# Kernel optimization log

Hardware: AMD Instinct MI355X
Metric: run time of the kernel (lower is better)

The kernel has to match this reference:

```python
import jax, jax.numpy as jnp
import numpy as np

WINDOW = 2  # window_size

def _causal_window_conv(x, W, b):
    # x: [B,T,D_in], W: [WINDOW, D_in, D_out], b: [D_out]
    # equivalent to left-padding x by WINDOW-1 zeros and a 'valid' conv
    B, T, _ = x.shape
    xp = jnp.pad(x, ((0, 0), (WINDOW - 1, 0), (0, 0)))  # [B, T+WINDOW-1, D_in]
    out = b
    for k in range(WINDOW):
        out = out + jnp.einsum('btd,de->bte', xp[:, k:k + T], W[k])
    return out  # [B,T,D_out]

def setup_inputs() -> dict:
    key = jax.random.key(0)
    ks = jax.random.split(key, 4)
    B, T, Din, Dout = 8, 4096, 256, 256
    scale = 0.05
    x = jax.random.normal(ks[0], (B, T, Din), dtype=jnp.float32)
    W_z = jax.random.normal(ks[1], (WINDOW, Din, Dout), dtype=jnp.float32) * scale
    W_f = jax.random.normal(ks[2], (WINDOW, Din, Dout), dtype=jnp.float32) * scale
    W_o = jax.random.normal(ks[3], (WINDOW, Din, Dout), dtype=jnp.float32) * scale
    b_z = jnp.zeros((Dout,), dtype=jnp.float32)
    b_f = jnp.zeros((Dout,), dtype=jnp.float32)
    b_o = jnp.zeros((Dout,), dtype=jnp.float32)
    return {"x": x, "W_z": W_z, "W_f": W_f, "W_o": W_o,
            "b_z": b_z, "b_f": b_f, "b_o": b_o}

def reference(x, W_z, W_f, W_o, b_z, b_f, b_o):
    # QRNN with fo-pooling (Bradbury et al. 2016), return_sequences=True
    z = jnp.tanh(_causal_window_conv(x, W_z, b_z))          # [B,T,D]
    f = jax.nn.sigmoid(_causal_window_conv(x, W_f, b_f))    # [B,T,D]
    o = jax.nn.sigmoid(_causal_window_conv(x, W_o, b_o))    # [B,T,D]

    def step(c, zfo):
        z_t, f_t, o_t = zfo
        c = f_t * c + (1.0 - f_t) * z_t   # fo-pooling recurrence
        h = o_t * c
        return c, h

    c0 = jnp.zeros(z.shape[::2], dtype=z.dtype)  # [B,D]
    # time-major for scan
    zfo = (z.transpose(1, 0, 2), f.transpose(1, 0, 2), o.transpose(1, 0, 2))
    _, hs = jax.lax.scan(step, c0, zfo)
    return hs.transpose(1, 0, 2)  # [B,T,D]
```

## Files before the change

### kernel.cpp

```cpp
#include <hip/hip_runtime.h>
#include <hip/hip_bf16.h>
#include <hip/hip_fp16.h>

#define BDIM 8
#define TDIM 4096
#define DDIM 256
#define MDIM (BDIM * TDIM)
#define NCHUNK 256
#define LCHUNK (TDIM / NCHUNK)

typedef _Float16 f16x8 __attribute__((ext_vector_type(8)));
typedef _Float16 f16x4 __attribute__((ext_vector_type(4)));
typedef float f32x4 __attribute__((ext_vector_type(4)));

__device__ __forceinline__ float sigmoid_(float x) {
    return 1.0f / (1.0f + __expf(-x));
}
__device__ __forceinline__ float tanh_(float x) {
    return 2.0f / (1.0f + __expf(-2.0f * x)) - 1.0f;
}

#define GLOAD_LDS16(g, l)                                                    \
    __builtin_amdgcn_global_load_lds(                                        \
        (const __attribute__((address_space(1))) void*)(g),                  \
        (__attribute__((address_space(3))) void*)(l), 16, 0, 0)

__global__ __launch_bounds__(256) void prep(
    const float* __restrict__ x, _Float16* __restrict__ xpad,
    const float* __restrict__ Wz, const float* __restrict__ Wf,
    const float* __restrict__ Wo, _Float16* __restrict__ Wt) {
    const int bx = blockIdx.x;
    if (bx < 1536) {
        const int idx = bx * 256 + threadIdx.x;
        const int n = idx & 255;
        const int kin = (idx >> 8) & 255;
        const int w = (idx >> 16) & 1;
        const int g = idx >> 17;
        const float* W = (g == 0) ? Wz : (g == 1) ? Wf : Wo;
        const float v = W[(size_t)w * 65536 + (size_t)kin * 256 + n];
        Wt[((size_t)g * 256 + n) * 512 + w * 256 + kin] = (_Float16)v;
        return;
    }
    const int bxx = bx - 1536;
    const int b = bxx / 1025;
    const int tb = bxx - b * 1025;
    const int tp = tb * 4 + (threadIdx.x >> 6);
    const int q = threadIdx.x & 63;
    if (tp > TDIM) return;
    float4 v = make_float4(0.f, 0.f, 0.f, 0.f);
    if (tp > 0)
        v = *(const float4*)(x + ((size_t)b * TDIM + tp - 1) * DDIM + q * 4);
    f16x4 h;
    h[0] = (_Float16)v.x; h[1] = (_Float16)v.y;
    h[2] = (_Float16)v.z; h[3] = (_Float16)v.w;
    *(f16x4*)(xpad + ((size_t)b * (TDIM + 1) + tp) * DDIM + q * 4) = h;
}

__global__ __launch_bounds__(256, 2) void gates_mfma(
    const _Float16* __restrict__ xpad, const _Float16* __restrict__ Wt,
    const float* __restrict__ bz, const float* __restrict__ bfv,
    const float* __restrict__ bo,
    _Float16* __restrict__ zbuf, _Float16* __restrict__ fbuf,
    _Float16* __restrict__ obuf) {
    const int hw = blockIdx.x;
    const int logical = (hw & 7) * 192 + (hw >> 3);
    const int mblk = logical / 6;
    const int rem = logical - mblk * 6;
    const int gate = rem % 3;
    const int nblk = rem / 3;
    const int m0 = mblk * 128;
    const int n0 = nblk * 128;

    const int tid = threadIdx.x;
    const int lane = tid & 63;
    const int wave = tid >> 6;
    const int wr = wave >> 1;
    const int wc = wave & 1;

    __shared__ __align__(16) char smem[65536];

    const int s = wave * 64 + lane;
    const int r1 = s >> 3;
    const int kc = (((s & 7) ^ ((s >> 3) & 7))) * 8;

    const int b = m0 >> 12;
    const int t0 = m0 & (TDIM - 1);

    const _Float16* srcA =
        xpad + ((size_t)b * (TDIM + 1) + t0 + r1) * DDIM + kc;
    const _Float16* srcB = Wt + ((size_t)gate * 256 + n0 + r1) * 512 + kc;

#define STAGE_(slot, kt)                                                     \
    {                                                                        \
        char* dA = smem + (slot) * 32768 + wave * 1024;                      \
        char* dB = smem + (slot) * 32768 + 16384 + wave * 1024;              \
        GLOAD_LDS16(srcA + (kt) * 64, dA);                                   \
        GLOAD_LDS16(srcA + (kt) * 64 + 32 * DDIM, dA + 4096);                \
        GLOAD_LDS16(srcA + (kt) * 64 + 64 * DDIM, dA + 8192);                \
        GLOAD_LDS16(srcA + (kt) * 64 + 96 * DDIM, dA + 12288);               \
        GLOAD_LDS16(srcB + (kt) * 64, dB);                                   \
        GLOAD_LDS16(srcB + (kt) * 64 + 32 * 512, dB + 4096);                 \
        GLOAD_LDS16(srcB + (kt) * 64 + 64 * 512, dB + 8192);                 \
        GLOAD_LDS16(srcB + (kt) * 64 + 96 * 512, dB + 12288);                \
    }

    f32x4 acc[4][4] = {};
    const int am = lane & 15;
    const int c0 = (((lane >> 4) ^ (lane & 7))) * 8;
    const int c1 = (((4 + (lane >> 4)) ^ (lane & 7))) * 8;

    STAGE_(0, 0);

#pragma unroll
    for (int t = 0; t < 8; ++t) {
        asm volatile("s_waitcnt vmcnt(0)" ::: "memory");
        __builtin_amdgcn_s_barrier();
        __builtin_amdgcn_sched_barrier(0);
        if (t < 7) STAGE_((t + 1) & 1, t + 1);

        const _Float16* Ab = (const _Float16*)(smem + (t & 1) * 32768);
        const _Float16* Bb = Ab + 8192;

        f16x8 a0[4], b0[4], a1[4], b1[4];
#pragma unroll
        for (int i = 0; i < 4; ++i)
            a0[i] = *(const f16x8*)(Ab + (wr * 64 + i * 16 + am) * 64 + c0);
#pragma unroll
        for (int j = 0; j < 4; ++j)
            b0[j] = *(const f16x8*)(Bb + (wc * 64 + j * 16 + am) * 64 + c0);
        __builtin_amdgcn_sched_barrier(0);
#pragma unroll
        for (int i = 0; i < 4; ++i)
            a1[i] = *(const f16x8*)(Ab + (wr * 64 + i * 16 + am) * 64 + c1);
#pragma unroll
        for (int j = 0; j < 4; ++j)
            b1[j] = *(const f16x8*)(Bb + (wc * 64 + j * 16 + am) * 64 + c1);

        asm volatile("s_waitcnt lgkmcnt(8)" ::: "memory");
        __builtin_amdgcn_sched_barrier(0);
        __builtin_amdgcn_s_setprio(1);
#pragma unroll
        for (int i = 0; i < 4; ++i)
#pragma unroll
            for (int j = 0; j < 4; ++j)
                acc[i][j] = __builtin_amdgcn_mfma_f32_16x16x32_f16(
                    b0[j], a0[i], acc[i][j], 0, 0, 0);
        __builtin_amdgcn_s_setprio(0);
        asm volatile("s_waitcnt lgkmcnt(0)" ::: "memory");
        __builtin_amdgcn_sched_barrier(0);
        __builtin_amdgcn_s_setprio(1);
#pragma unroll
        for (int i = 0; i < 4; ++i)
#pragma unroll
            for (int j = 0; j < 4; ++j)
                acc[i][j] = __builtin_amdgcn_mfma_f32_16x16x32_f16(
                    b1[j], a1[i], acc[i][j], 0, 0, 0);
        __builtin_amdgcn_s_setprio(0);
    }
#undef STAGE_

    const float* bias = (gate == 0) ? bz : (gate == 1) ? bfv : bo;
    _Float16* outp = (gate == 0) ? zbuf : (gate == 1) ? fbuf : obuf;
    const int nq = (lane >> 4) * 4;
#pragma unroll
    for (int i = 0; i < 4; ++i) {
        const size_t gm = (size_t)(m0 + wr * 64 + i * 16 + am);
#pragma unroll
        for (int j = 0; j < 4; ++j) {
            const int gc = n0 + wc * 64 + j * 16 + nq;
            const float4 b4 = *(const float4*)(bias + gc);
            f32x4 v = acc[i][j];
            f16x4 h;
            if (gate == 0) {
                h[0] = (_Float16)tanh_(v[0] + b4.x);
                h[1] = (_Float16)tanh_(v[1] + b4.y);
                h[2] = (_Float16)tanh_(v[2] + b4.z);
                h[3] = (_Float16)tanh_(v[3] + b4.w);
            } else {
                h[0] = (_Float16)sigmoid_(v[0] + b4.x);
                h[1] = (_Float16)sigmoid_(v[1] + b4.y);
                h[2] = (_Float16)sigmoid_(v[2] + b4.z);
                h[3] = (_Float16)sigmoid_(v[3] + b4.w);
            }
            *(f16x4*)(outp + gm * DDIM + gc) = h;
        }
    }
}

__global__ __launch_bounds__(256) void scan_pass1(
    const _Float16* __restrict__ zbuf, const _Float16* __restrict__ fbuf,
    float* __restrict__ aggA, float* __restrict__ aggB) {
    const int idx = blockIdx.x * 256 + threadIdx.x;
    const int d4 = idx & 63;
    const int chunk = (idx >> 6) & (NCHUNK - 1);
    const int b = idx >> 14;

    const size_t row0 = (size_t)b * TDIM + (size_t)chunk * LCHUNK;
    const int2* zp = (const int2*)zbuf + row0 * 64 + d4;
    const int2* fp = (const int2*)fbuf + row0 * 64 + d4;

    float A[4], c[4];
#pragma unroll
    for (int e = 0; e < 4; ++e) { A[e] = 1.0f; c[e] = 0.0f; }

    for (int i = 0; i < LCHUNK; ++i) {
        int2 fv = *fp;
        int2 zv = *zp;
        const _Float16* fh = (const _Float16*)&fv;
        const _Float16* zh = (const _Float16*)&zv;
#pragma unroll
        for (int e = 0; e < 4; ++e) {
            const float f = (float)fh[e];
            const float z = (float)zh[e];
            A[e] *= f;
            c[e] = f * c[e] + (1.0f - f) * z;
        }
        fp += 64;
        zp += 64;
    }
    ((float4*)aggA)[idx] = make_float4(A[0], A[1], A[2], A[3]);
    ((float4*)aggB)[idx] = make_float4(c[0], c[1], c[2], c[3]);
}

__global__ __launch_bounds__(256) void carry_scan(
    const float* __restrict__ aggA, const float* __restrict__ aggB,
    float* __restrict__ carry) {
    const int g = blockIdx.x * 256 + threadIdx.x;
    const int d = g & 255;
    const int b = g >> 8;
    const size_t base = (size_t)b * NCHUNK * 256 + d;

    float c = 0.0f;
    for (int ch0 = 0; ch0 < NCHUNK; ch0 += 16) {
        float A[16], Bv[16];
#pragma unroll
        for (int u = 0; u < 16; ++u) {
            const size_t p = base + (size_t)(ch0 + u) * 256;
            A[u] = aggA[p];
            Bv[u] = aggB[p];
        }
#pragma unroll
        for (int u = 0; u < 16; ++u) {
            const size_t p = base + (size_t)(ch0 + u) * 256;
            carry[p] = c;
            c = A[u] * c + Bv[u];
        }
    }
}

__global__ __launch_bounds__(256) void scan_pass2(
    const _Float16* __restrict__ zbuf, const _Float16* __restrict__ fbuf,
    const _Float16* __restrict__ obuf, const float* __restrict__ carry,
    float* __restrict__ out) {
    const int idx = blockIdx.x * 256 + threadIdx.x;
    const int d4 = idx & 63;
    const int chunk = (idx >> 6) & (NCHUNK - 1);
    const int b = idx >> 14;

    float c[4];
    const float4 c0 = ((const float4*)carry)[idx];
    c[0] = c0.x; c[1] = c0.y; c[2] = c0.z; c[3] = c0.w;

    const size_t row0 = (size_t)b * TDIM + (size_t)chunk * LCHUNK;
    const int2* zp = (const int2*)zbuf + row0 * 64 + d4;
    const int2* fp = (const int2*)fbuf + row0 * 64 + d4;
    const int2* op = (const int2*)obuf + row0 * 64 + d4;
    float4* hp = (float4*)out + row0 * 64 + d4;

    for (int i = 0; i < LCHUNK; ++i) {
        int2 fv = *fp;
        int2 zv = *zp;
        int2 ov = *op;
        const _Float16* fh = (const _Float16*)&fv;
        const _Float16* zh = (const _Float16*)&zv;
        const _Float16* oh = (const _Float16*)&ov;
        float h[4];
#pragma unroll
        for (int e = 0; e < 4; ++e) {
            const float f = (float)fh[e];
            const float z = (float)zh[e];
            c[e] = f * c[e] + (1.0f - f) * z;
            h[e] = (float)oh[e] * c[e];
        }
        *hp = make_float4(h[0], h[1], h[2], h[3]);
        fp += 64;
        zp += 64;
        op += 64;
        hp += 64;
    }
}

extern "C" void kernel_launch(void* const* d_in, const int* in_sizes, int n_in,
                              void* d_out, int out_size, void* d_ws,
                              size_t ws_size, hipStream_t stream) {
    const float* x = (const float*)d_in[0];
    const float* Wz = (const float*)d_in[1];
    const float* Wf = (const float*)d_in[2];
    const float* Wo = (const float*)d_in[3];
    const float* bz = (const float*)d_in[4];
    const float* bfv = (const float*)d_in[5];
    const float* bo = (const float*)d_in[6];
    float* out = (float*)d_out;

    char* p = (char*)d_ws;
    _Float16* xpad = (_Float16*)p;  p += (size_t)BDIM * (TDIM + 1) * DDIM * 2;
    _Float16* Wt = (_Float16*)p;    p += (size_t)3 * 256 * 512 * 2;
    _Float16* zbuf = (_Float16*)p;  p += (size_t)MDIM * DDIM * 2;
    _Float16* fbuf = (_Float16*)p;  p += (size_t)MDIM * DDIM * 2;
    _Float16* obuf = (_Float16*)p;  p += (size_t)MDIM * DDIM * 2;
    float* aggA = (float*)p;        p += (size_t)BDIM * NCHUNK * DDIM * 4;
    float* aggB = (float*)p;        p += (size_t)BDIM * NCHUNK * DDIM * 4;
    float* carry = (float*)p;

    prep<<<1536 + 1025 * BDIM, 256, 0, stream>>>(x, xpad, Wz, Wf, Wo, Wt);

    gates_mfma<<<MDIM / 128 * (DDIM / 128) * 3, 256, 0, stream>>>(
        xpad, Wt, bz, bfv, bo, zbuf, fbuf, obuf);

    scan_pass1<<<(BDIM * NCHUNK * 64) / 256, 256, 0, stream>>>(zbuf, fbuf,
                                                               aggA, aggB);
    carry_scan<<<(BDIM * DDIM) / 256, 256, 0, stream>>>(aggA, aggB, carry);
    scan_pass2<<<(BDIM * NCHUNK * 64) / 256, 256, 0, stream>>>(zbuf, fbuf,
                                                               obuf, carry, out);
}
```

Before: 159.3 us.

## Widen gate GEMM tile to full 256 columns with 512 threads and triple-buffered LDS

```diff
diff --git a/kernel.cpp b/kernel.cpp
--- a/kernel.cpp
+++ b/kernel.cpp
@@ -56,52 +56,46 @@
     *(f16x4*)(xpad + ((size_t)b * (TDIM + 1) + tp) * DDIM + q * 4) = h;
 }
 
-__global__ __launch_bounds__(256, 2) void gates_mfma(
+__global__ __launch_bounds__(512, 2) void gates_mfma(
     const _Float16* __restrict__ xpad, const _Float16* __restrict__ Wt,
     const float* __restrict__ bz, const float* __restrict__ bfv,
     const float* __restrict__ bo,
     _Float16* __restrict__ zbuf, _Float16* __restrict__ fbuf,
     _Float16* __restrict__ obuf) {
     const int hw = blockIdx.x;
-    const int logical = (hw & 7) * 192 + (hw >> 3);
-    const int mblk = logical / 6;
-    const int rem = logical - mblk * 6;
-    const int gate = rem % 3;
-    const int nblk = rem / 3;
+    const int logical = (hw & 7) * 96 + (hw >> 3);
+    const int mblk = logical / 3;
+    const int gate = logical - mblk * 3;
     const int m0 = mblk * 128;
-    const int n0 = nblk * 128;
 
     const int tid = threadIdx.x;
     const int lane = tid & 63;
     const int wave = tid >> 6;
-    const int wr = wave >> 1;
-    const int wc = wave & 1;
-
-    __shared__ __align__(16) char smem[65536];
-
-    const int s = wave * 64 + lane;
-    const int r1 = s >> 3;
-    const int kc = (((s & 7) ^ ((s >> 3) & 7))) * 8;
+    const int wm = wave >> 2;
+    const int wn = wave & 3;
+
+    __shared__ __align__(16) char smem[147456];
+
+    const int r1 = tid >> 3;
+    const int kc = (((tid & 7) ^ ((tid >> 3) & 7))) * 8;
 
     const int b = m0 >> 12;
     const int t0 = m0 & (TDIM - 1);
 
     const _Float16* srcA =
         xpad + ((size_t)b * (TDIM + 1) + t0 + r1) * DDIM + kc;
-    const _Float16* srcB = Wt + ((size_t)gate * 256 + n0 + r1) * 512 + kc;
+    const _Float16* srcB = Wt + ((size_t)gate * 256 + r1) * 512 + kc;
 
 #define STAGE_(slot, kt)                                                     \
     {                                                                        \
-        char* dA = smem + (slot) * 32768 + wave * 1024;                      \
-        char* dB = smem + (slot) * 32768 + 16384 + wave * 1024;              \
+        char* dA = smem + (slot) * 49152 + tid * 16;                         \
+        char* dB = smem + (slot) * 49152 + 16384 + tid * 16;                 \
         GLOAD_LDS16(srcA + (kt) * 64, dA);                                   \
-        GLOAD_LDS16(srcA + (kt) * 64 + 32 * DDIM, dA + 4096);                \
         GLOAD_LDS16(srcA + (kt) * 64 + 64 * DDIM, dA + 8192);                \
-        GLOAD_LDS16(srcA + (kt) * 64 + 96 * DDIM, dA + 12288);               \
         GLOAD_LDS16(srcB + (kt) * 64, dB);                                   \
-        GLOAD_LDS16(srcB + (kt) * 64 + 32 * 512, dB + 4096);                 \
         GLOAD_LDS16(srcB + (kt) * 64 + 64 * 512, dB + 8192);                 \
-        GLOAD_LDS16(srcB + (kt) * 64 + 96 * 512, dB + 12288);                \
+        GLOAD_LDS16(srcB + (kt) * 64 + 128 * 512, dB + 16384);               \
+        GLOAD_LDS16(srcB + (kt) * 64 + 192 * 512, dB + 24576);               \
     }
 
     f32x4 acc[4][4] = {};
@@ -110,31 +104,36 @@
     const int c1 = (((4 + (lane >> 4)) ^ (lane & 7))) * 8;
 
     STAGE_(0, 0);
+    STAGE_(1, 1);
 
 #pragma unroll
     for (int t = 0; t < 8; ++t) {
-        asm volatile("s_waitcnt vmcnt(0)" ::: "memory");
+        if (t < 7)
+            asm volatile("s_waitcnt vmcnt(6)" ::: "memory");
+        else
+            asm volatile("s_waitcnt vmcnt(0)" ::: "memory");
         __builtin_amdgcn_s_barrier();
         __builtin_amdgcn_sched_barrier(0);
-        if (t < 7) STAGE_((t + 1) & 1, t + 1);
-
-        const _Float16* Ab = (const _Float16*)(smem + (t & 1) * 32768);
-        const _Float16* Bb = Ab + 8192;
+        if (t < 6) STAGE_((t + 2) % 3, t + 2);
+
+        const _Float16* Ab = (const _Float16*)(smem + (t % 3) * 49152);
+        const _Float16* Bb =
+            (const _Float16*)(smem + (t % 3) * 49152 + 16384);
 
         f16x8 a0[4], b0[4], a1[4], b1[4];
 #pragma unroll
         for (int i = 0; i < 4; ++i)
-            a0[i] = *(const f16x8*)(Ab + (wr * 64 + i * 16 + am) * 64 + c0);
+            a0[i] = *(const f16x8*)(Ab + (wm * 64 + i * 16 + am) * 64 + c0);
 #pragma unroll
         for (int j = 0; j < 4; ++j)
-            b0[j] = *(const f16x8*)(Bb + (wc * 64 + j * 16 + am) * 64 + c0);
+            b0[j] = *(const f16x8*)(Bb + (wn * 64 + j * 16 + am) * 64 + c0);
         __builtin_amdgcn_sched_barrier(0);
 #pragma unroll
         for (int i = 0; i < 4; ++i)
-            a1[i] = *(const f16x8*)(Ab + (wr * 64 + i * 16 + am) * 64 + c1);
+            a1[i] = *(const f16x8*)(Ab + (wm * 64 + i * 16 + am) * 64 + c1);
 #pragma unroll
         for (int j = 0; j < 4; ++j)
-            b1[j] = *(const f16x8*)(Bb + (wc * 64 + j * 16 + am) * 64 + c1);
+            b1[j] = *(const f16x8*)(Bb + (wn * 64 + j * 16 + am) * 64 + c1);
 
         asm volatile("s_waitcnt lgkmcnt(8)" ::: "memory");
         __builtin_amdgcn_sched_barrier(0);
@@ -164,10 +163,10 @@
     const int nq = (lane >> 4) * 4;
 #pragma unroll
     for (int i = 0; i < 4; ++i) {
-        const size_t gm = (size_t)(m0 + wr * 64 + i * 16 + am);
+        const size_t gm = (size_t)(m0 + wm * 64 + i * 16 + am);
 #pragma unroll
         for (int j = 0; j < 4; ++j) {
-            const int gc = n0 + wc * 64 + j * 16 + nq;
+            const int gc = wn * 64 + j * 16 + nq;
             const float4 b4 = *(const float4*)(bias + gc);
             f32x4 v = acc[i][j];
             f16x4 h;
@@ -314,8 +313,8 @@
 
     prep<<<1536 + 1025 * BDIM, 256, 0, stream>>>(x, xpad, Wz, Wf, Wo, Wt);
 
-    gates_mfma<<<MDIM / 128 * (DDIM / 128) * 3, 256, 0, stream>>>(
-        xpad, Wt, bz, bfv, bo, zbuf, fbuf, obuf);
+    gates_mfma<<<768, 512, 0, stream>>>(xpad, Wt, bz, bfv, bo,
+                                        zbuf, fbuf, obuf);
 
     scan_pass1<<<(BDIM * NCHUNK * 64) / 256, 256, 0, stream>>>(zbuf, fbuf,
                                                                aggA, aggB);
```

Result: no change. 160.2 us (+0.6%).
